# Kernel optimization log

Measured on AMD Instinct MI355X. Metric: run time of the kernel, lower is better.

Reference implementation:

```python
import jax, jax.numpy as jnp
import numpy as np
import math

B, S, D, H, DFF, L = 8, 1024, 512, 8, 2048, 4
DK = D // H
EPS = 1e-5
NEG = -1e32


def _sinusoidal_pe(s, d):
    pos = np.arange(s)[:, None].astype(np.float32)
    div = np.exp(np.arange(0, d, 2).astype(np.float32) * (-math.log(10000.0) / d))
    pe = np.zeros((s, d), np.float32)
    pe[:, 0::2] = np.sin(pos * div)
    pe[:, 1::2] = np.cos(pos * div)
    return jnp.asarray(pe)


def setup_inputs() -> dict:
    key = jax.random.key(0)
    ks = jax.random.split(key, 20)
    sd = 0.02
    inp = {
        "q_embed_data": jax.random.normal(ks[0], (B, S, D), jnp.float32),
        "qa_embed_data": jax.random.normal(ks[1], (B, S, D), jnp.float32),
        "pe": _sinusoidal_pe(S, D),
        # stacked per-layer params (leading dim L). kq_same=1 -> q uses Wk.
        "Wk": sd * jax.random.normal(ks[2], (L, D, D), jnp.float32),
        "bk": jnp.zeros((L, D), jnp.float32),
        "Wv": sd * jax.random.normal(ks[3], (L, D, D), jnp.float32),
        "bv": jnp.zeros((L, D), jnp.float32),
        "Wo": sd * jax.random.normal(ks[4], (L, D, D), jnp.float32),
        "bo": jnp.zeros((L, D), jnp.float32),
        "ln1_s": jnp.ones((L, D), jnp.float32),
        "ln1_b": jnp.zeros((L, D), jnp.float32),
        "W1": sd * jax.random.normal(ks[5], (L, D, DFF), jnp.float32),
        "b1": jnp.zeros((L, DFF), jnp.float32),
        "W2": sd * jax.random.normal(ks[6], (L, DFF, D), jnp.float32),
        "b2": jnp.zeros((L, D), jnp.float32),
        "ln2_s": jnp.ones((L, D), jnp.float32),
        "ln2_b": jnp.zeros((L, D), jnp.float32),
    }
    return inp


def _layernorm(z, s, b):
    m = z.mean(-1, keepdims=True)
    v = ((z - m) ** 2).mean(-1, keepdims=True)
    return (z - m) / jnp.sqrt(v + EPS) * s + b


def _forward(q_embed_data, qa_embed_data, pe, Wk, bk, Wv, bv, Wo, bo,
             ln1_s, ln1_b, W1, b1, W2, b2, ln2_s, ln2_b):
    x = q_embed_data + pe[None, :, :]
    y = qa_embed_data + pe[None, :, :]  # values source stays fixed across blocks
    allowed = jnp.tril(jnp.ones((S, S), bool), -1)  # strictly-causal: attend only to j < i
    row_keep = (jnp.arange(S) > 0).astype(x.dtype)[None, None, :, None]  # zero_pad row 0

    def heads(z, W, b):
        return (z @ W + b).reshape(B, S, H, DK).transpose(0, 2, 1, 3)  # [B,H,S,DK]

    def step(xc, p):
        wk, bk_, wv, bv_, wo, bo_, s1, b1n, w1, b1f, w2, b2f, s2, b2n = p
        q = heads(xc, wk, bk_)  # kq_same: q via k_linear
        k = heads(xc, wk, bk_)
        v = heads(y, wv, bv_)
        sc = jnp.einsum('bhid,bhjd->bhij', q, k) / math.sqrt(DK)
        att = jax.nn.softmax(jnp.where(allowed, sc, NEG), axis=-1) * row_keep
        o = jnp.einsum('bhij,bhjd->bhid', att, v).transpose(0, 2, 1, 3).reshape(B, S, D)
        x1 = _layernorm(xc + (o @ wo + bo_), s1, b1n)
        f = jax.nn.relu(x1 @ w1 + b1f) @ w2 + b2f
        x2 = _layernorm(x1 + f, s2, b2n)
        return x2, None

    out, _ = jax.lax.scan(step, x, (Wk, bk, Wv, bv, Wo, bo, ln1_s, ln1_b, W1, b1, W2, b2, ln2_s, ln2_b))
    return out


def reference(q_embed_data, qa_embed_data, pe, Wk, bk, Wv, bv, Wo, bo,
              ln1_s, ln1_b, W1, b1, W2, b2, ln2_s, ln2_b):
    return _forward(q_embed_data, qa_embed_data, pe, Wk, bk, Wv, bv, Wo, bo,
                    ln1_s, ln1_b, W1, b1, W2, b2, ln2_s, ln2_b)
```

## Files before the change

### kernel.cpp

```cpp
#include <hip/hip_runtime.h>
#include <stdint.h>

typedef __attribute__((ext_vector_type(8))) __bf16 bf16x8;
typedef __attribute__((ext_vector_type(4))) float f32x4;
typedef __attribute__((ext_vector_type(4))) unsigned int u32x4;

constexpr int B = 8, S = 1024, D = 512, H = 8, DFF = 2048, L = 4, DK = 64;
constexpr int MR = B * S;
constexpr int NSLOT = 80;

__device__ __forceinline__ unsigned short f2bf(float f) {
    union { float f; unsigned u; } v; v.f = f;
    unsigned u = v.u;
    u += 0x7fffu + ((u >> 16) & 1u);
    return (unsigned short)(u >> 16);
}

__device__ __forceinline__ void gload_lds16(const void* g, void* l) {
    __builtin_amdgcn_global_load_lds(
        (const __attribute__((address_space(1))) void*)g,
        (__attribute__((address_space(3))) void*)l, 16, 0, 0);
}

__global__ __launch_bounds__(256) void add_pe_kernel(
    const float* __restrict__ qe, const float* __restrict__ qa,
    const float* __restrict__ pe, float* __restrict__ x_f32,
    unsigned short* __restrict__ x_bf, unsigned short* __restrict__ y_bf) {
    int gid = blockIdx.x * 256 + threadIdx.x;
    int base = gid * 4;
    int po = base & (S * D - 1);
    float4 p = *(const float4*)(pe + po);
    float4 a = *(const float4*)(qe + base);
    float4 q = *(const float4*)(qa + base);
    float4 xv = make_float4(a.x + p.x, a.y + p.y, a.z + p.z, a.w + p.w);
    float4 yv = make_float4(q.x + p.x, q.y + p.y, q.z + p.z, q.w + p.w);
    *(float4*)(x_f32 + base) = xv;
    ushort4 xb; xb.x = f2bf(xv.x); xb.y = f2bf(xv.y); xb.z = f2bf(xv.z); xb.w = f2bf(xv.w);
    ushort4 yb; yb.x = f2bf(yv.x); yb.y = f2bf(yv.y); yb.z = f2bf(yv.z); yb.w = f2bf(yv.w);
    *(ushort4*)(x_bf + base) = xb;
    *(ushort4*)(y_bf + base) = yb;
}

__global__ __launch_bounds__(256) void wtrans_kernel(
    const float* __restrict__ src, unsigned short* __restrict__ dst, int K, int N) {
    __shared__ float t[64][65];
    src += (size_t)blockIdx.z * K * N;
    dst += (size_t)blockIdx.z * K * N;
    int n0 = blockIdx.x * 64, k0 = blockIdx.y * 64;
    int tid = threadIdx.x;
    int r = tid >> 4, c4 = (tid & 15) * 4;
    #pragma unroll
    for (int rr = 0; rr < 64; rr += 16) {
        float4 v = *(const float4*)(src + (size_t)(k0 + r + rr) * N + n0 + c4);
        t[r + rr][c4] = v.x; t[r + rr][c4 + 1] = v.y;
        t[r + rr][c4 + 2] = v.z; t[r + rr][c4 + 3] = v.w;
    }
    __syncthreads();
    int n = tid >> 2, kc = (tid & 3) * 16;
    ushort4 o[4];
    #pragma unroll
    for (int g = 0; g < 4; g++) {
        o[g].x = f2bf(t[kc + g * 4 + 0][n]);
        o[g].y = f2bf(t[kc + g * 4 + 1][n]);
        o[g].z = f2bf(t[kc + g * 4 + 2][n]);
        o[g].w = f2bf(t[kc + g * 4 + 3][n]);
    }
    unsigned short* dp = dst + (size_t)(n0 + n) * K + k0 + kc;
    #pragma unroll
    for (int g = 0; g < 4; g++) *(ushort4*)(dp + g * 4) = o[g];
}

template<int BN, bool RELU, bool RESID, bool OUT_F32, bool OUT_BF16, bool OUT_VT>
__global__ __launch_bounds__(256) void gemm_kernel(
    const unsigned short* __restrict__ A, const unsigned short* __restrict__ Bt,
    const float* __restrict__ bias, const float* __restrict__ resid,
    float* __restrict__ out_f32, unsigned short* __restrict__ out_bf,
    int M, int N, int K) {
    constexpr int MT = (BN == 128) ? 4 : 2;
    constexpr int WROWS = (BN == 128) ? 64 : 32;
    constexpr int BRND = (BN == 128) ? 4 : 2;
    __shared__ unsigned short a_lds[128 * 64];
    __shared__ unsigned short b_lds[BN * 64];

    const int tid = threadIdx.x;
    const int lane = tid & 63, wid = tid >> 6;
    const int wm = (BN == 128) ? (wid >> 1) : wid;
    const int wn = (BN == 128) ? (wid & 1) : 0;
    const int l15 = lane & 15, quad = lane >> 4;
    const int nmt = gridDim.x, nnt = gridDim.y;
    const int o_lin = blockIdx.y * nmt + blockIdx.x;
    const int xcd = o_lin & 7, oi = o_lin >> 3;
    const int mtile = xcd * (nmt >> 3) + oi / nnt;
    const int ntile = oi % nnt;
    const int m0 = mtile * 128, n0 = ntile * BN;

    f32x4 acc[MT][4];
    #pragma unroll
    for (int i = 0; i < MT; i++)
        #pragma unroll
        for (int j = 0; j < 4; j++) { f32x4 z = {0.f, 0.f, 0.f, 0.f}; acc[i][j] = z; }

    const unsigned short* aP[4];
    unsigned short* aL[4];
    #pragma unroll
    for (int j = 0; j < 4; j++) {
        int c = wid * 256 + j * 64 + lane;
        int r = c >> 3, slot = c & 7, kg = slot ^ (r & 7);
        aP[j] = A + (size_t)(m0 + r) * K + kg * 8;
        aL[j] = a_lds + (size_t)(wid * 256 + j * 64) * 8;
    }
    const unsigned short* bP[BRND];
    unsigned short* bL[BRND];
    #pragma unroll
    for (int j = 0; j < BRND; j++) {
        int c = wid * (BRND * 64) + j * 64 + lane;
        int r = c >> 3, slot = c & 7, kg = slot ^ (r & 7);
        bP[j] = Bt + (size_t)(n0 + r) * K + kg * 8;
        bL[j] = b_lds + (size_t)(wid * (BRND * 64) + j * 64) * 8;
    }

    for (int k0 = 0; k0 < K; k0 += 64) {
        #pragma unroll
        for (int j = 0; j < 4; j++) gload_lds16(aP[j] + k0, aL[j]);
        #pragma unroll
        for (int j = 0; j < BRND; j++) gload_lds16(bP[j] + k0, bL[j]);
        __syncthreads();

        bf16x8 af[MT][2], bfv[4][2];
        #pragma unroll
        for (int mt = 0; mt < MT; mt++) {
            int row = wm * WROWS + mt * 16 + l15;
            #pragma unroll
            for (int kh = 0; kh < 2; kh++)
                af[mt][kh] = *(const bf16x8*)&a_lds[row * 64 + (((kh * 4 + quad) ^ (row & 7)) * 8)];
        }
        #pragma unroll
        for (int nt = 0; nt < 4; nt++) {
            int row = wn * 64 + nt * 16 + l15;
            #pragma unroll
            for (int kh = 0; kh < 2; kh++)
                bfv[nt][kh] = *(const bf16x8*)&b_lds[row * 64 + (((kh * 4 + quad) ^ (row & 7)) * 8)];
        }
        #pragma unroll
        for (int mt = 0; mt < MT; mt++)
            #pragma unroll
            for (int nt = 0; nt < 4; nt++) {
                acc[mt][nt] = __builtin_amdgcn_mfma_f32_16x16x32_bf16(af[mt][0], bfv[nt][0], acc[mt][nt], 0, 0, 0);
                acc[mt][nt] = __builtin_amdgcn_mfma_f32_16x16x32_bf16(af[mt][1], bfv[nt][1], acc[mt][nt], 0, 0, 0);
            }
        __syncthreads();
    }

    #pragma unroll
    for (int nt = 0; nt < 4; nt++) {
        int col = n0 + wn * 64 + nt * 16 + l15;
        float bv = bias[col];
        #pragma unroll
        for (int mt = 0; mt < MT; mt++) {
            int row0 = m0 + wm * WROWS + mt * 16 + quad * 4;
            if (OUT_VT) {
                int hh = col >> 6, d = col & 63;
                int bb = row0 >> 10, s0 = row0 & 1023;
                ushort4 o;
                o.x = f2bf(acc[mt][nt][0] + bv);
                o.y = f2bf(acc[mt][nt][1] + bv);
                o.z = f2bf(acc[mt][nt][2] + bv);
                o.w = f2bf(acc[mt][nt][3] + bv);
                *(ushort4*)(out_bf + ((size_t)(bb * H + hh) * DK + d) * S + s0) = o;
            } else {
                #pragma unroll
                for (int r = 0; r < 4; r++) {
                    int row = row0 + r;
                    float v = acc[mt][nt][r] + bv;
                    if (RESID) v += resid[(size_t)row * N + col];
                    if (RELU) v = fmaxf(v, 0.f);
                    size_t o = (size_t)row * N + col;
                    if (OUT_F32) out_f32[o] = v;
                    if (OUT_BF16) out_bf[o] = f2bf(v);
                }
            }
        }
    }
}

__global__ __launch_bounds__(256) void ln_kernel(
    const float* __restrict__ in, const float* __restrict__ gamma,
    const float* __restrict__ beta, float* __restrict__ out_f32,
    unsigned short* __restrict__ out_bf) {
    __shared__ float red[8];
    int row = blockIdx.x, tid = threadIdx.x;
    const float* p = in + (size_t)row * D;
    float2 v = *(const float2*)(p + tid * 2);
    float s = v.x + v.y;
    float q = v.x * v.x + v.y * v.y;
    #pragma unroll
    for (int off = 32; off > 0; off >>= 1) {
        s += __shfl_xor(s, off);
        q += __shfl_xor(q, off);
    }
    int wid = tid >> 6, lane = tid & 63;
    if (lane == 0) { red[wid] = s; red[4 + wid] = q; }
    __syncthreads();
    s = red[0] + red[1] + red[2] + red[3];
    q = red[4] + red[5] + red[6] + red[7];
    float mean = s * (1.f / D);
    float var = q * (1.f / D) - mean * mean;
    float inv = rsqrtf(var + 1e-5f);
    int c = tid * 2;
    float2 g = *(const float2*)(gamma + c);
    float2 bb = *(const float2*)(beta + c);
    float o0 = (v.x - mean) * inv * g.x + bb.x;
    float o1 = (v.y - mean) * inv * g.y + bb.y;
    *(float2*)(out_f32 + (size_t)row * D + c) = make_float2(o0, o1);
    ushort2 ob; ob.x = f2bf(o0); ob.y = f2bf(o1);
    *(ushort2*)(out_bf + (size_t)row * D + c) = ob;
}

__global__ __launch_bounds__(256, 2) void attn_part_kernel(
    const unsigned short* __restrict__ qk, const unsigned short* __restrict__ vt,
    float* __restrict__ part_o, float* __restrict__ part_l) {
    __shared__ unsigned short kbuf[2][64 * 64];
    __shared__ unsigned short vbuf[2][64 * 64];
    __shared__ unsigned p_u32[4][32 * 36];
    constexpr float C = 0.18033688011112042f;
    const float NEGINF = -__builtin_huge_valf();

    const int bx = blockIdx.x;
    const int e = 19 - (bx >> 6);
    const int hh = bx & 63;
    const int b = hh >> 3, h = hh & 7;
    const int head = hh;
    const int tid = threadIdx.x;
    const int w = tid >> 6, lane = tid & 63;
    const int l15 = lane & 15, quad = lane >> 4;

    int Qb, st;
    if (e >= 16)     { Qb = 7; st = 16; }
    else if (e >= 12){ Qb = 6; st = 12; }
    else if (e >= 9) { Qb = 5; st = 9;  }
    else if (e >= 6) { Qb = 4; st = 6;  }
    else if (e >= 4) { Qb = 3; st = 4;  }
    else if (e >= 2) { Qb = 2; st = 2;  }
    else             { Qb = e; st = e;  }
    const int c = e - st;
    const int nc = (Qb >> 1) + 1;
    const int nkt = (Qb + 1) * 2;
    const int ck0 = (c * nkt) / nc, ck1 = ((c + 1) * nkt) / nc;
    const int qrow0 = Qb * 128 + w * 32;

    const int rowbase = b * S, colbase = h * DK;
    const unsigned short* kbase = qk + (size_t)rowbase * D + colbase;
    const unsigned short* vbase = vt + (size_t)head * (DK * S);

    bf16x8 qf[2][2];
    #pragma unroll
    for (int u = 0; u < 2; u++) {
        const unsigned short* qrow =
            qk + (size_t)(rowbase + qrow0 + u * 16 + l15) * D + colbase;
        qf[u][0] = *(const bf16x8*)(qrow + quad * 8);
        qf[u][1] = *(const bf16x8*)(qrow + 32 + quad * 8);
    }

    const int sr = lane >> 3;
    const int sseg = (lane & 7) ^ sr;
    const unsigned short* kgp[2]; const unsigned short* vgp[2];
    unsigned short* kld[2]; unsigned short* vld[2];
    #pragma unroll
    for (int j = 0; j < 2; j++) {
        int rt = w * 16 + j * 8 + sr;
        kgp[j] = kbase + (size_t)rt * D + sseg * 8;
        vgp[j] = vbase + (size_t)rt * S + sseg * 8;
        kld[j] = &kbuf[0][(w * 16 + j * 8) * 64];
        vld[j] = &vbuf[0][(w * 16 + j * 8) * 64];
    }
    auto stage = [&](int buf, int kt) {
        #pragma unroll
        for (int j = 0; j < 2; j++) gload_lds16(kgp[j] + (size_t)kt * 64 * D, kld[j] + buf * 4096);
        #pragma unroll
        for (int j = 0; j < 2; j++) gload_lds16(vgp[j] + kt * 64, vld[j] + buf * 4096);
    };

    float l_r[2] = {0.f, 0.f};
    f32x4 o_acc[2][4];
    #pragma unroll
    for (int u = 0; u < 2; u++)
        #pragma unroll
        for (int i = 0; i < 4; i++) { f32x4 z = {0.f, 0.f, 0.f, 0.f}; o_acc[u][i] = z; }

    auto consume = [&](int kt, const unsigned short* kl, const unsigned short* vl) {
        unsigned* pb = p_u32[w];
        bf16x8 kf[4][2];
        #pragma unroll
        for (int mt = 0; mt < 4; mt++) {
            const unsigned short* kr = kl + (mt * 16 + l15) * 64;
            #pragma unroll
            for (int kh = 0; kh < 2; kh++)
                kf[mt][kh] = *(const bf16x8*)(kr + (((kh * 4 + quad) ^ (l15 & 7)) * 8));
        }
        const bool diag = kt * 64 + 64 > qrow0;
        #pragma unroll
        for (int u = 0; u < 2; u++) {
            const int qb = qrow0 + u * 16;
            const int ql = u * 16 + l15;
            #pragma unroll
            for (int mt = 0; mt < 4; mt++) {
                if (kt * 64 + mt * 16 < qb + 16) {
                    f32x4 a = {0.f, 0.f, 0.f, 0.f};
                    a = __builtin_amdgcn_mfma_f32_16x16x32_bf16(kf[mt][0], qf[u][0], a, 0, 0, 0);
                    a = __builtin_amdgcn_mfma_f32_16x16x32_bf16(kf[mt][1], qf[u][1], a, 0, 0, 0);
                    if (diag) {
                        const int gi = qb + l15;
                        #pragma unroll
                        for (int r = 0; r < 4; r++) {
                            int gj = kt * 64 + mt * 16 + quad * 4 + r;
                            a[r] = (gj >= gi) ? NEGINF : a[r];
                        }
                    }
                    float e0 = exp2f(a[0] * C), e1 = exp2f(a[1] * C);
                    float e2 = exp2f(a[2] * C), e3 = exp2f(a[3] * C);
                    unsigned pk0, pk1;
                    asm("v_cvt_pk_bf16_f32 %0, %1, %2" : "=v"(pk0) : "v"(e0), "v"(e1));
                    asm("v_cvt_pk_bf16_f32 %0, %1, %2" : "=v"(pk1) : "v"(e2), "v"(e3));
                    l_r[u] += (e0 + e1) + (e2 + e3);
                    *(uint2*)&pb[ql * 36 + mt * 8 + quad * 2] = make_uint2(pk0, pk1);
                } else {
                    *(uint2*)&pb[ql * 36 + mt * 8 + quad * 2] = make_uint2(0u, 0u);
                }
            }
        }
        bf16x8 vf[4][2];
        #pragma unroll
        for (int mt = 0; mt < 4; mt++) {
            const unsigned short* vr = vl + (mt * 16 + l15) * 64;
            #pragma unroll
            for (int kh = 0; kh < 2; kh++)
                vf[mt][kh] = *(const bf16x8*)(vr + (((kh * 4 + quad) ^ (l15 & 7)) * 8));
        }
        #pragma unroll
        for (int u = 0; u < 2; u++) {
            const int qb = qrow0 + u * 16;
            const int ql = u * 16 + l15;
            u32x4 d0 = *(const u32x4*)&pb[ql * 36 + quad * 4];
            bf16x8 pb0 = __builtin_bit_cast(bf16x8, d0);
            const bool hi = (kt * 64 + 32 < qb + 16);
            if (hi) {
                u32x4 d1 = *(const u32x4*)&pb[ql * 36 + 16 + quad * 4];
                bf16x8 pb1 = __builtin_bit_cast(bf16x8, d1);
                #pragma unroll
                for (int mt = 0; mt < 4; mt++) {
                    o_acc[u][mt] = __builtin_amdgcn_mfma_f32_16x16x32_bf16(vf[mt][0], pb0, o_acc[u][mt], 0, 0, 0);
                    o_acc[u][mt] = __builtin_amdgcn_mfma_f32_16x16x32_bf16(vf[mt][1], pb1, o_acc[u][mt], 0, 0, 0);
                }
            } else {
                #pragma unroll
                for (int mt = 0; mt < 4; mt++)
                    o_acc[u][mt] = __builtin_amdgcn_mfma_f32_16x16x32_bf16(vf[mt][0], pb0, o_acc[u][mt], 0, 0, 0);
            }
        }
    };

    stage(0, ck0);
    for (int kt = ck0; kt < ck1; ++kt) {
        const int cur = (kt - ck0) & 1;
        if (kt + 1 < ck1) {
            stage(cur ^ 1, kt + 1);
            asm volatile("s_waitcnt vmcnt(4)" ::: "memory");
        } else {
            asm volatile("s_waitcnt vmcnt(0)" ::: "memory");
        }
        __builtin_amdgcn_sched_barrier(0);
        __builtin_amdgcn_s_barrier();
        __builtin_amdgcn_sched_barrier(0);
        if (kt * 64 < qrow0 + 32)
            consume(kt, &kbuf[cur][0], &vbuf[cur][0]);
        __builtin_amdgcn_sched_barrier(0);
        __builtin_amdgcn_s_barrier();
        __builtin_amdgcn_sched_barrier(0);
    }

    #pragma unroll
    for (int u = 0; u < 2; u++) {
        l_r[u] += __shfl_xor(l_r[u], 16);
        l_r[u] += __shfl_xor(l_r[u], 32);
    }

    const int p = head * NSLOT + 4 * st + c * 4 + w;
    if (quad == 0) {
        #pragma unroll
        for (int u = 0; u < 2; u++)
            part_l[(size_t)p * 32 + u * 16 + l15] = l_r[u];
    }
    float* po = part_o + (size_t)p * 2048;
    #pragma unroll
    for (int u = 0; u < 2; u++)
        #pragma unroll
        for (int mt = 0; mt < 4; mt++)
            #pragma unroll
            for (int r = 0; r < 4; r++)
                po[(mt * 16 + quad * 4 + r) * 32 + u * 16 + l15] = o_acc[u][mt][r];
}

__global__ __launch_bounds__(256) void attn_combine_kernel(
    const float* __restrict__ part_o, const float* __restrict__ part_l,
    unsigned short* __restrict__ ob) {
    int bx = blockIdx.x;
    int t = bx & 31, head = bx >> 5;
    int b = head >> 3, h = head & 7;
    int tid = threadIdx.x;
    int q = tid >> 3, dg = (tid & 7) * 8;
    int Qb = t >> 2, w = t & 3;
    int nc = (Qb >> 1) + 1;
    int m = Qb >> 1;
    int st = m * m + ((Qb & 1) ? Qb : m);
    int p0 = head * NSLOT + 4 * st + w;

    float ldenom = 0.f;
    for (int c = 0; c < nc; c++)
        ldenom += part_l[(size_t)(p0 + 4 * c) * 32 + q];
    float inv = (ldenom > 0.f) ? 1.f / ldenom : 0.f;
    int si = t * 32 + q;
    if (si == 0) inv = 0.f;

    float v[8] = {0.f, 0.f, 0.f, 0.f, 0.f, 0.f, 0.f, 0.f};
    for (int c = 0; c < nc; c++) {
        const float* po = part_o + (size_t)(p0 + 4 * c) * 2048;
        #pragma unroll
        for (int i = 0; i < 8; i++)
            v[i] += po[(dg + i) * 32 + q];
    }
    unsigned short out[8];
    #pragma unroll
    for (int i = 0; i < 8; i++) out[i] = f2bf(v[i] * inv);
    unsigned short* dst = ob + (size_t)(b * S + si) * D + h * DK + dg;
    *(u32x4*)dst = *(const u32x4*)out;
}

extern "C" void kernel_launch(void* const* d_in, const int* in_sizes, int n_in,
                              void* d_out, int out_size, void* d_ws, size_t ws_size,
                              hipStream_t stream) {
    (void)in_sizes; (void)n_in; (void)out_size; (void)ws_size;
    const float* qe  = (const float*)d_in[0];
    const float* qa  = (const float*)d_in[1];
    const float* pe  = (const float*)d_in[2];
    const float* Wk  = (const float*)d_in[3];
    const float* bk  = (const float*)d_in[4];
    const float* Wv  = (const float*)d_in[5];
    const float* bv  = (const float*)d_in[6];
    const float* Wo  = (const float*)d_in[7];
    const float* bo  = (const float*)d_in[8];
    const float* l1s = (const float*)d_in[9];
    const float* l1b = (const float*)d_in[10];
    const float* W1  = (const float*)d_in[11];
    const float* b1  = (const float*)d_in[12];
    const float* W2  = (const float*)d_in[13];
    const float* b2  = (const float*)d_in[14];
    const float* l2s = (const float*)d_in[15];
    const float* l2b = (const float*)d_in[16];

    char* w = (char*)d_ws;
    float* x_f32  = (float*)w;           w += (size_t)MR * D * 4;
    float* t_f32  = (float*)w;           w += (size_t)MR * D * 4;
    float* x1_f32 = (float*)w;           w += (size_t)MR * D * 4;
    unsigned short* x_bf  = (unsigned short*)w; w += (size_t)MR * D * 2;
    unsigned short* y_bf  = (unsigned short*)w; w += (size_t)MR * D * 2;
    unsigned short* qk_bf = (unsigned short*)w; w += (size_t)MR * D * 2;
    unsigned short* vt_bf = (unsigned short*)w; w += (size_t)MR * D * 2;
    unsigned short* o_bf  = (unsigned short*)w; w += (size_t)MR * D * 2;
    unsigned short* x1_bf = (unsigned short*)w; w += (size_t)MR * D * 2;
    char* scratch = w;                          w += (size_t)NSLOT * 64 * 2048 * 4;
    unsigned short* h_bf = (unsigned short*)scratch;
    float* part_o = (float*)scratch;
    unsigned short* wkT = (unsigned short*)w;   w += (size_t)L * D * D * 2;
    unsigned short* wvT = (unsigned short*)w;   w += (size_t)L * D * D * 2;
    unsigned short* woT = (unsigned short*)w;   w += (size_t)L * D * D * 2;
    unsigned short* w1T = (unsigned short*)w;   w += (size_t)L * D * DFF * 2;
    unsigned short* w2T = (unsigned short*)w;   w += (size_t)L * DFF * D * 2;
    float* part_l = (float*)w;                  w += (size_t)NSLOT * 64 * 32 * 4;

    add_pe_kernel<<<MR * D / 4 / 256, 256, 0, stream>>>(qe, qa, pe, x_f32, x_bf, y_bf);
    wtrans_kernel<<<dim3(8, 8, L), 256, 0, stream>>>(Wk, wkT, D, D);
    wtrans_kernel<<<dim3(8, 8, L), 256, 0, stream>>>(Wv, wvT, D, D);
    wtrans_kernel<<<dim3(8, 8, L), 256, 0, stream>>>(Wo, woT, D, D);
    wtrans_kernel<<<dim3(32, 8, L), 256, 0, stream>>>(W1, w1T, D, DFF);
    wtrans_kernel<<<dim3(8, 32, L), 256, 0, stream>>>(W2, w2T, DFF, D);

    dim3 g512(64, 8), g2048(64, 16);
    for (int l = 0; l < L; l++) {
        gemm_kernel<64, false, false, false, true, false><<<g512, 256, 0, stream>>>(
            x_bf, wkT + (size_t)l * D * D, bk + l * D, nullptr, nullptr, qk_bf, MR, D, D);
        gemm_kernel<64, false, false, false, false, true><<<g512, 256, 0, stream>>>(
            y_bf, wvT + (size_t)l * D * D, bv + l * D, nullptr, nullptr, vt_bf, MR, D, D);
        attn_part_kernel<<<20 * 64, 256, 0, stream>>>(qk_bf, vt_bf, part_o, part_l);
        attn_combine_kernel<<<64 * 32, 256, 0, stream>>>(part_o, part_l, o_bf);
        gemm_kernel<64, false, true, true, false, false><<<g512, 256, 0, stream>>>(
            o_bf, woT + (size_t)l * D * D, bo + l * D, x_f32, t_f32, nullptr, MR, D, D);
        ln_kernel<<<MR, 256, 0, stream>>>(t_f32, l1s + l * D, l1b + l * D, x1_f32, x1_bf);
        gemm_kernel<128, true, false, false, true, false><<<g2048, 256, 0, stream>>>(
            x1_bf, w1T + (size_t)l * D * DFF, b1 + l * DFF, nullptr, nullptr, h_bf, MR, DFF, D);
        gemm_kernel<64, false, true, true, false, false><<<g512, 256, 0, stream>>>(
            h_bf, w2T + (size_t)l * DFF * D, b2 + l * D, x1_f32, t_f32, nullptr, MR, D, DFF);
        float* xo = (l == L - 1) ? (float*)d_out : x_f32;
        ln_kernel<<<MR, 256, 0, stream>>>(t_f32, l2s + l * D, l2b + l * D, xo, x_bf);
    }
}
```

Before: 771.2 us.

## Fuse Q/K and V projections into one launch and drop attention split-K combine

Merges the two projection GEMMs (x·Wk and y·Wv) into one kernel launch, with blockIdx.z choosing the operand set. The attention kernel no longer splits the key range across several blocks. Each block now handles a whole 128-row query block and normalizes its output directly, which removes the fp32 partial buffers and the separate combine kernel. The trade-off is worse load balance: causal blocks now range from 2 to 16 key tiles, and there are only 512 blocks instead of 1280, so the largest blocks may set the tail latency.

```diff
diff --git a/kernel.cpp b/kernel.cpp
--- a/kernel.cpp
+++ b/kernel.cpp
@@ -7,7 +7,6 @@
 
 constexpr int B = 8, S = 1024, D = 512, H = 8, DFF = 2048, L = 4, DK = 64;
 constexpr int MR = B * S;
-constexpr int NSLOT = 80;
 
 __device__ __forceinline__ unsigned short f2bf(float f) {
     union { float f; unsigned u; } v; v.f = f;
@@ -183,6 +182,114 @@
     }
 }
 
+__global__ __launch_bounds__(256) void gemm_qkv_kernel(
+    const unsigned short* __restrict__ x_bf, const unsigned short* __restrict__ y_bf,
+    const unsigned short* __restrict__ wkT, const unsigned short* __restrict__ wvT,
+    const float* __restrict__ bk, const float* __restrict__ bv,
+    unsigned short* __restrict__ qk_out, unsigned short* __restrict__ vt_out) {
+    constexpr int BN = 64, MT = 2, WROWS = 32, BRND = 2;
+    constexpr int N = 512, K = 512;
+    __shared__ unsigned short a_lds[128 * 64];
+    __shared__ unsigned short b_lds[BN * 64];
+
+    const bool isv = blockIdx.z != 0;
+    const unsigned short* A  = isv ? y_bf : x_bf;
+    const unsigned short* Bt = isv ? wvT : wkT;
+    const float* bias        = isv ? bv : bk;
+
+    const int tid = threadIdx.x;
+    const int lane = tid & 63, wid = tid >> 6;
+    const int l15 = lane & 15, quad = lane >> 4;
+    const int nmt = gridDim.x, nnt = gridDim.y;
+    const int o_lin = blockIdx.y * nmt + blockIdx.x;
+    const int xcd = o_lin & 7, oi = o_lin >> 3;
+    const int mtile = xcd * (nmt >> 3) + oi / nnt;
+    const int ntile = oi % nnt;
+    const int m0 = mtile * 128, n0 = ntile * BN;
+
+    f32x4 acc[MT][4];
+    #pragma unroll
+    for (int i = 0; i < MT; i++)
+        #pragma unroll
+        for (int j = 0; j < 4; j++) { f32x4 z = {0.f, 0.f, 0.f, 0.f}; acc[i][j] = z; }
+
+    const unsigned short* aP[4];
+    unsigned short* aL[4];
+    #pragma unroll
+    for (int j = 0; j < 4; j++) {
+        int c = wid * 256 + j * 64 + lane;
+        int r = c >> 3, slot = c & 7, kg = slot ^ (r & 7);
+        aP[j] = A + (size_t)(m0 + r) * K + kg * 8;
+        aL[j] = a_lds + (size_t)(wid * 256 + j * 64) * 8;
+    }
+    const unsigned short* bP[BRND];
+    unsigned short* bL[BRND];
+    #pragma unroll
+    for (int j = 0; j < BRND; j++) {
+        int c = wid * (BRND * 64) + j * 64 + lane;
+        int r = c >> 3, slot = c & 7, kg = slot ^ (r & 7);
+        bP[j] = Bt + (size_t)(n0 + r) * K + kg * 8;
+        bL[j] = b_lds + (size_t)(wid * (BRND * 64) + j * 64) * 8;
+    }
+
+    for (int k0 = 0; k0 < K; k0 += 64) {
+        #pragma unroll
+        for (int j = 0; j < 4; j++) gload_lds16(aP[j] + k0, aL[j]);
+        #pragma unroll
+        for (int j = 0; j < BRND; j++) gload_lds16(bP[j] + k0, bL[j]);
+        __syncthreads();
+
+        bf16x8 af[MT][2], bfv[4][2];
+        #pragma unroll
+        for (int mt = 0; mt < MT; mt++) {
+            int row = wid * WROWS + mt * 16 + l15;
+            #pragma unroll
+            for (int kh = 0; kh < 2; kh++)
+                af[mt][kh] = *(const bf16x8*)&a_lds[row * 64 + (((kh * 4 + quad) ^ (row & 7)) * 8)];
+        }
+        #pragma unroll
+        for (int nt = 0; nt < 4; nt++) {
+            int row = nt * 16 + l15;
+            #pragma unroll
+            for (int kh = 0; kh < 2; kh++)
+                bfv[nt][kh] = *(const bf16x8*)&b_lds[row * 64 + (((kh * 4 + quad) ^ (row & 7)) * 8)];
+        }
+        #pragma unroll
+        for (int mt = 0; mt < MT; mt++)
+            #pragma unroll
+            for (int nt = 0; nt < 4; nt++) {
+                acc[mt][nt] = __builtin_amdgcn_mfma_f32_16x16x32_bf16(af[mt][0], bfv[nt][0], acc[mt][nt], 0, 0, 0);
+                acc[mt][nt] = __builtin_amdgcn_mfma_f32_16x16x32_bf16(af[mt][1], bfv[nt][1], acc[mt][nt], 0, 0, 0);
+            }
+        __syncthreads();
+    }
+
+    #pragma unroll
+    for (int nt = 0; nt < 4; nt++) {
+        int col = n0 + nt * 16 + l15;
+        float bv_ = bias[col];
+        #pragma unroll
+        for (int mt = 0; mt < MT; mt++) {
+            int row0 = m0 + wid * WROWS + mt * 16 + quad * 4;
+            ushort4 o;
+            o.x = f2bf(acc[mt][nt][0] + bv_);
+            o.y = f2bf(acc[mt][nt][1] + bv_);
+            o.z = f2bf(acc[mt][nt][2] + bv_);
+            o.w = f2bf(acc[mt][nt][3] + bv_);
+            if (isv) {
+                int hh = col >> 6, d = col & 63;
+                int bb = row0 >> 10, s0 = row0 & 1023;
+                *(ushort4*)(vt_out + ((size_t)(bb * H + hh) * DK + d) * S + s0) = o;
+            } else {
+                #pragma unroll
+                for (int r = 0; r < 4; r++)
+                    qk_out[(size_t)(row0 + r) * N + col] =
+                        (r == 0) ? o.x : (r == 1) ? o.y : (r == 2) ? o.z : o.w;
+            }
+        }
+    }
+}
+
 __global__ __launch_bounds__(256) void ln_kernel(
     const float* __restrict__ in, const float* __restrict__ gamma,
     const float* __restrict__ beta, float* __restrict__ out_f32,
@@ -216,9 +323,9 @@
     *(ushort2*)(out_bf + (size_t)row * D + c) = ob;
 }
 
-__global__ __launch_bounds__(256, 2) void attn_part_kernel(
+__global__ __launch_bounds__(256, 2) void attn_kernel(
     const unsigned short* __restrict__ qk, const unsigned short* __restrict__ vt,
-    float* __restrict__ part_o, float* __restrict__ part_l) {
+    unsigned short* __restrict__ ob) {
     __shared__ unsigned short kbuf[2][64 * 64];
     __shared__ unsigned short vbuf[2][64 * 64];
     __shared__ unsigned p_u32[4][32 * 36];
@@ -226,7 +333,7 @@
     const float NEGINF = -__builtin_huge_valf();
 
     const int bx = blockIdx.x;
-    const int e = 19 - (bx >> 6);
+    const int Qb = 7 - (bx >> 6);
     const int hh = bx & 63;
     const int b = hh >> 3, h = hh & 7;
     const int head = hh;
@@ -234,18 +341,7 @@
     const int w = tid >> 6, lane = tid & 63;
     const int l15 = lane & 15, quad = lane >> 4;
 
-    int Qb, st;
-    if (e >= 16)     { Qb = 7; st = 16; }
-    else if (e >= 12){ Qb = 6; st = 12; }
-    else if (e >= 9) { Qb = 5; st = 9;  }
-    else if (e >= 6) { Qb = 4; st = 6;  }
-    else if (e >= 4) { Qb = 3; st = 4;  }
-    else if (e >= 2) { Qb = 2; st = 2;  }
-    else             { Qb = e; st = e;  }
-    const int c = e - st;
-    const int nc = (Qb >> 1) + 1;
-    const int nkt = (Qb + 1) * 2;
-    const int ck0 = (c * nkt) / nc, ck1 = ((c + 1) * nkt) / nc;
+    const int nkt = 2 * Qb + 2;
     const int qrow0 = Qb * 128 + w * 32;
 
     const int rowbase = b * S, colbase = h * DK;
@@ -359,10 +455,10 @@
         }
     };
 
-    stage(0, ck0);
-    for (int kt = ck0; kt < ck1; ++kt) {
-        const int cur = (kt - ck0) & 1;
-        if (kt + 1 < ck1) {
+    stage(0, 0);
+    for (int kt = 0; kt < nkt; ++kt) {
+        const int cur = kt & 1;
+        if (kt + 1 < nkt) {
             stage(cur ^ 1, kt + 1);
             asm volatile("s_waitcnt vmcnt(4)" ::: "memory");
         } else {
@@ -383,56 +479,22 @@
         l_r[u] += __shfl_xor(l_r[u], 16);
         l_r[u] += __shfl_xor(l_r[u], 32);
     }
-
-    const int p = head * NSLOT + 4 * st + c * 4 + w;
-    if (quad == 0) {
-        #pragma unroll
-        for (int u = 0; u < 2; u++)
-            part_l[(size_t)p * 32 + u * 16 + l15] = l_r[u];
-    }
-    float* po = part_o + (size_t)p * 2048;
-    #pragma unroll
-    for (int u = 0; u < 2; u++)
-        #pragma unroll
-        for (int mt = 0; mt < 4; mt++)
-            #pragma unroll
-            for (int r = 0; r < 4; r++)
-                po[(mt * 16 + quad * 4 + r) * 32 + u * 16 + l15] = o_acc[u][mt][r];
-}
-
-__global__ __launch_bounds__(256) void attn_combine_kernel(
-    const float* __restrict__ part_o, const float* __restrict__ part_l,
-    unsigned short* __restrict__ ob) {
-    int bx = blockIdx.x;
-    int t = bx & 31, head = bx >> 5;
-    int b = head >> 3, h = head & 7;
-    int tid = threadIdx.x;
-    int q = tid >> 3, dg = (tid & 7) * 8;
-    int Qb = t >> 2, w = t & 3;
-    int nc = (Qb >> 1) + 1;
-    int m = Qb >> 1;
-    int st = m * m + ((Qb & 1) ? Qb : m);
-    int p0 = head * NSLOT + 4 * st + w;
-
-    float ldenom = 0.f;
-    for (int c = 0; c < nc; c++)
-        ldenom += part_l[(size_t)(p0 + 4 * c) * 32 + q];
-    float inv = (ldenom > 0.f) ? 1.f / ldenom : 0.f;
-    int si = t * 32 + q;
-    if (si == 0) inv = 0.f;
-
-    float v[8] = {0.f, 0.f, 0.f, 0.f, 0.f, 0.f, 0.f, 0.f};
-    for (int c = 0; c < nc; c++) {
-        const float* po = part_o + (size_t)(p0 + 4 * c) * 2048;
-        #pragma unroll
-        for (int i = 0; i < 8; i++)
-            v[i] += po[(dg + i) * 32 + q];
-    }
-    unsigned short out[8];
-    #pragma unroll
-    for (int i = 0; i < 8; i++) out[i] = f2bf(v[i] * inv);
-    unsigned short* dst = ob + (size_t)(b * S + si) * D + h * DK + dg;
-    *(u32x4*)dst = *(const u32x4*)out;
+    #pragma unroll
+    for (int u = 0; u < 2; u++) {
+        const int si = qrow0 + u * 16 + l15;
+        float inv = (l_r[u] > 0.f) ? 1.f / l_r[u] : 0.f;
+        if (si == 0) inv = 0.f;
+        unsigned short* orow = ob + (size_t)(b * S + si) * D + h * DK;
+        #pragma unroll
+        for (int mt = 0; mt < 4; mt++) {
+            ushort4 o;
+            o.x = f2bf(o_acc[u][mt][0] * inv);
+            o.y = f2bf(o_acc[u][mt][1] * inv);
+            o.z = f2bf(o_acc[u][mt][2] * inv);
+            o.w = f2bf(o_acc[u][mt][3] * inv);
+            *(ushort4*)(orow + mt * 16 + quad * 4) = o;
+        }
+    }
 }
 
 extern "C" void kernel_launch(void* const* d_in, const int* in_sizes, int n_in,
@@ -467,15 +529,12 @@
     unsigned short* vt_bf = (unsigned short*)w; w += (size_t)MR * D * 2;
     unsigned short* o_bf  = (unsigned short*)w; w += (size_t)MR * D * 2;
     unsigned short* x1_bf = (unsigned short*)w; w += (size_t)MR * D * 2;
-    char* scratch = w;                          w += (size_t)NSLOT * 64 * 2048 * 4;
-    unsigned short* h_bf = (unsigned short*)scratch;
-    float* part_o = (float*)scratch;
+    unsigned short* h_bf  = (unsigned short*)w; w += (size_t)MR * DFF * 2;
     unsigned short* wkT = (unsigned short*)w;   w += (size_t)L * D * D * 2;
     unsigned short* wvT = (unsigned short*)w;   w += (size_t)L * D * D * 2;
     unsigned short* woT = (unsigned short*)w;   w += (size_t)L * D * D * 2;
     unsigned short* w1T = (unsigned short*)w;   w += (size_t)L * D * DFF * 2;
     unsigned short* w2T = (unsigned short*)w;   w += (size_t)L * DFF * D * 2;
-    float* part_l = (float*)w;                  w += (size_t)NSLOT * 64 * 32 * 4;
 
     add_pe_kernel<<<MR * D / 4 / 256, 256, 0, stream>>>(qe, qa, pe, x_f32, x_bf, y_bf);
     wtrans_kernel<<<dim3(8, 8, L), 256, 0, stream>>>(Wk, wkT, D, D);
@@ -486,12 +545,10 @@
 
     dim3 g512(64, 8), g2048(64, 16);
     for (int l = 0; l < L; l++) {
-        gemm_kernel<64, false, false, false, true, false><<<g512, 256, 0, stream>>>(
-            x_bf, wkT + (size_t)l * D * D, bk + l * D, nullptr, nullptr, qk_bf, MR, D, D);
-        gemm_kernel<64, false, false, false, false, true><<<g512, 256, 0, stream>>>(
-            y_bf, wvT + (size_t)l * D * D, bv + l * D, nullptr, nullptr, vt_bf, MR, D, D);
-        attn_part_kernel<<<20 * 64, 256, 0, stream>>>(qk_bf, vt_bf, part_o, part_l);
-        attn_combine_kernel<<<64 * 32, 256, 0, stream>>>(part_o, part_l, o_bf);
+        gemm_qkv_kernel<<<dim3(64, 8, 2), 256, 0, stream>>>(
+            x_bf, y_bf, wkT + (size_t)l * D * D, wvT + (size_t)l * D * D,
+            bk + l * D, bv + l * D, qk_bf, vt_bf);
+        attn_kernel<<<512, 256, 0, stream>>>(qk_bf, vt_bf, o_bf);
         gemm_kernel<64, false, true, true, false, false><<<g512, 256, 0, stream>>>(
             o_bf, woT + (size_t)l * D * D, bo + l * D, x_f32, t_f32, nullptr, MR, D, D);
         ln_kernel<<<MR, 256, 0, stream>>>(t_f32, l1s + l * D, l1b + l * D, x1_f32, x1_bf);
```

Result: faster. 718.6 us, median of 2 (-6.8%).
